# Optimization experiments

Measured on AMD Instinct MI355X. Metric: run time of the kernel, lower is better.

The kernel has to match this reference:

```python
import jax, jax.numpy as jnp
import numpy as np

N_EVENTS = 16
N_SAMPLES = 2 ** 15  # 32768


def fft_shift(stems, shift_samples):
    """Fractionally shift each atom in time via frequency-domain phase rotation.
    stems: (B, E, N) float32; shift_samples: (B, E) float32 in [0, N].
    """
    n = stems.shape[-1]
    freqs = jnp.fft.rfftfreq(n).astype(jnp.float32)  # (n//2+1,) cycles/sample
    theta = 2.0 * jnp.pi * freqs[None, None, :] * shift_samples[..., None]  # (B,E,F)
    phase = jnp.cos(theta) - 1j * jnp.sin(theta)  # exp(-i*theta)
    spec = jnp.fft.rfft(stems, axis=-1)
    return jnp.fft.irfft(spec * phase, n=n, axis=-1)


def setup_inputs() -> dict:
    key = jax.random.key(0)
    k1, k2, k3, k4 = jax.random.split(key, 4)
    B = 64
    time_latent = jax.random.normal(k1, (B, N_EVENTS, 128), dtype=jnp.float32)
    stems = jax.random.normal(k2, (B, N_EVENTS, N_SAMPLES), dtype=jnp.float32)
    targets = jax.random.normal(k3, (B, 1, N_SAMPLES), dtype=jnp.float32)
    W_pos = jax.random.normal(k4, (1, 128), dtype=jnp.float32) * 0.1
    b_pos = jnp.zeros((1,), dtype=jnp.float32)
    return {"time_latent": time_latent, "stems": stems, "targets": targets,
            "W_pos": W_pos, "b_pos": b_pos}


def reference(time_latent, stems, targets, W_pos, b_pos):
    # to_pos: Linear(128 -> 1), then sigmoid -> fractional positions in [0,1]
    pos = jax.nn.sigmoid(jnp.einsum('bed,od->beo', time_latent, W_pos) + b_pos)
    pos = pos.reshape(-1, N_EVENTS)  # (B, E)
    # schedule_atoms: place each stem at fractional offset pos * n_samples, sum events
    shifted = fft_shift(stems, pos * N_SAMPLES)  # (B, E, N)
    scheduled = jnp.sum(shifted, axis=1, keepdims=True)  # (B, 1, N), same shape as targets
    return scheduled
```

## Files before the change

kernel.cpp:

```cpp
#include <hip/hip_runtime.h>
#include <math.h>

#define NS      32768
#define M       16384
#define NEV     16
#define NB      64
#define T2      1024

__device__ __forceinline__ int ldsIdx(int i) { return i + (i >> 5) + (i >> 10); }
#define LDS_ELEMS (M + M / 32 + M / 1024)

__device__ __forceinline__ float2 cmul(float2 a, float2 b) {
    return make_float2(a.x * b.x - a.y * b.y, a.x * b.y + a.y * b.x);
}

__device__ __forceinline__ int rev4_14(int i) {
    int r = 0;
#pragma unroll
    for (int d = 0; d < 7; ++d) { r = (r << 2) | (i & 3); i >>= 2; }
    return r;
}

__device__ __forceinline__ float2 shift_phase(int k, int si, float sf) {
    unsigned ksi = ((unsigned)k * (unsigned)si) & (unsigned)(NS - 1);
    float total = (float)ksi + (float)k * sf;
    float f = total * (1.0f / (float)NS);
    f -= floorf(f);
    float ang = -6.28318530717958647692f * f;
    float sv, cv;
    __sincosf(ang, &sv, &cv);
    return make_float2(cv, sv);
}

__device__ __forceinline__ float2 wNS(int k) {
    float ang = (float)k * (-6.28318530717958647692f / (float)NS);
    float sv, cv;
    __sincosf(ang, &sv, &cv);
    return make_float2(cv, sv);
}

template <int SIGN>
__device__ void fft_lds(float2* lds, int tid) {
#pragma unroll
    for (int t = 0; t < 7; ++t) {
        const int q = 1 << (2 * t);
        const float c = (SIGN < 0 ? -6.28318530717958647692f
                                  :  6.28318530717958647692f) / (float)(4 * q);
#pragma unroll
        for (int it = 0; it < (M / 4) / T2; ++it) {
            const int bf = tid + it * T2;
            const int g = bf >> (2 * t);
            const int j = bf & (q - 1);
            const int base = (g << (2 * t + 2)) + j;
            const int I0 = ldsIdx(base);
            const int I1 = ldsIdx(base + q);
            const int I2 = ldsIdx(base + 2 * q);
            const int I3 = ldsIdx(base + 3 * q);
            float2 a0 = lds[I0];
            float2 a1 = lds[I1];
            float2 a2 = lds[I2];
            float2 a3 = lds[I3];
            if (q != 1) {
                float sv, cv;
                __sincosf(c * (float)j, &sv, &cv);
                float2 w1 = make_float2(cv, sv);
                float2 w2 = cmul(w1, w1);
                float2 w3 = cmul(w2, w1);
                a1 = cmul(a1, w1);
                a2 = cmul(a2, w2);
                a3 = cmul(a3, w3);
            }
            float2 u0 = make_float2(a0.x + a2.x, a0.y + a2.y);
            float2 u1 = make_float2(a0.x - a2.x, a0.y - a2.y);
            float2 u2 = make_float2(a1.x + a3.x, a1.y + a3.y);
            float2 u3 = make_float2(a1.x - a3.x, a1.y - a3.y);
            lds[I0] = make_float2(u0.x + u2.x, u0.y + u2.y);
            lds[I2] = make_float2(u0.x - u2.x, u0.y - u2.y);
            if (SIGN < 0) {
                lds[I1] = make_float2(u1.x + u3.y, u1.y - u3.x);
                lds[I3] = make_float2(u1.x - u3.y, u1.y + u3.x);
            } else {
                lds[I1] = make_float2(u1.x - u3.y, u1.y + u3.x);
                lds[I3] = make_float2(u1.x + u3.y, u1.y - u3.x);
            }
        }
        __syncthreads();
    }
}

__global__ __launch_bounds__(64) void pos_kernel(const float* __restrict__ tl,
                                                 const float* __restrict__ W,
                                                 const float* __restrict__ bp,
                                                 float* __restrict__ shifts) {
    int bid = blockIdx.x;
    int t = threadIdx.x;
    const float* row = tl + (size_t)bid * 128;
    float p = row[t] * W[t] + row[t + 64] * W[t + 64];
#pragma unroll
    for (int off = 32; off > 0; off >>= 1) p += __shfl_down(p, off);
    if (t == 0) {
        float x = p + bp[0];
        float sig = 1.0f / (1.0f + expf(-x));
        shifts[bid] = sig * (float)NS;
    }
}

__global__ __launch_bounds__(T2) void fft_phase_kernel(float* __restrict__ stems,
                                                       const float* __restrict__ shifts) {
    __shared__ float2 lds[LDS_ELEMS];
    const int tid = threadIdx.x;
    const int row = blockIdx.x;

    float* rowp = stems + (size_t)row * NS;
    const float4* src = (const float4*)rowp;
#pragma unroll
    for (int it = 0; it < (M / 2) / T2; ++it) {
        int i = tid + it * T2;
        float4 v = src[i];
        lds[ldsIdx(rev4_14(2 * i))]     = make_float2(v.x, v.y);
        lds[ldsIdx(rev4_14(2 * i + 1))] = make_float2(v.z, v.w);
    }
    __syncthreads();

    fft_lds<-1>(lds, tid);

    const float s = shifts[row];
    const int si = (int)floorf(s);
    const float sf = s - (float)si;
    float2* spec = (float2*)rowp;
#pragma unroll
    for (int t = 0; t < M / T2; ++t) {
        int k = tid + (t << 10);
        if (k == 0) {
            float2 z0 = lds[ldsIdx(0)];
            float X0 = z0.x + z0.y;
            float XM = z0.x - z0.y;
            float2 phM = shift_phase(M, si, sf);
            spec[0] = make_float2(X0, XM * phM.x);
        } else {
            float2 Zk = lds[ldsIdx(k)];
            float2 Zr = lds[ldsIdx(M - k)];
            float2 E = make_float2(0.5f * (Zk.x + Zr.x), 0.5f * (Zk.y - Zr.y));
            float2 O = make_float2(0.5f * (Zk.y + Zr.y), -0.5f * (Zk.x - Zr.x));
            float2 w = wNS(k);
            float2 wo = cmul(w, O);
            float2 X = make_float2(E.x + wo.x, E.y + wo.y);
            float2 ph = shift_phase(k, si, sf);
            spec[k] = cmul(X, ph);
        }
    }
}

__global__ __launch_bounds__(256) void reduce_kernel(const float4* __restrict__ stems,
                                                     float4* __restrict__ out) {
    int gid = blockIdx.x * 256 + threadIdx.x;
    int b = gid >> 13;
    int i = gid & (NS / 4 - 1);
    const float4* base = stems + (size_t)b * NEV * (NS / 4) + i;
    float4 s = base[0];
#pragma unroll
    for (int e = 1; e < NEV; ++e) {
        float4 v = base[(size_t)e * (NS / 4)];
        s.x += v.x; s.y += v.y; s.z += v.z; s.w += v.w;
    }
    out[gid] = s;
}

__global__ __launch_bounds__(T2) void inv_kernel(float* __restrict__ out) {
    __shared__ float2 lds[LDS_ELEMS];
    const int tid = threadIdx.x;
    const int b = blockIdx.x;

    const float4* src = (const float4*)(out + (size_t)b * NS);
#pragma unroll
    for (int it = 0; it < (M / 2) / T2; ++it) {
        int i = tid + it * T2;
        float4 v = src[i];
        lds[ldsIdx(rev4_14(2 * i))]     = make_float2(v.x, v.y);
        lds[ldsIdx(rev4_14(2 * i + 1))] = make_float2(v.z, v.w);
    }
    __syncthreads();

#pragma unroll
    for (int t = 0; t < (M / 2) / T2; ++t) {
        int k = tid + (t << 10);
        if (k == 0) {
            float2 a0 = lds[ldsIdx(0)];
            lds[ldsIdx(0)] = make_float2(0.5f * (a0.x + a0.y), 0.5f * (a0.x - a0.y));
            int rh = ldsIdx(rev4_14(M / 2));
            float2 ah = lds[rh];
            lds[rh] = make_float2(ah.x, -ah.y);
        } else {
            int pk = ldsIdx(rev4_14(k));
            int pm = ldsIdx(rev4_14(M - k));
            float2 a = lds[pk];
            float2 bb = lds[pm];
            float2 w = wNS(k);
            float2 E1 = make_float2(0.5f * (a.x + bb.x), 0.5f * (a.y - bb.y));
            float2 D1 = make_float2(0.5f * (a.x - bb.x), 0.5f * (a.y + bb.y));
            float2 wc = make_float2(w.x, -w.y);
            float2 O1 = cmul(wc, D1);
            float2 z1 = make_float2(E1.x - O1.y, E1.y + O1.x);
            float2 E2 = make_float2(E1.x, -E1.y);
            float2 D2 = make_float2(-D1.x, D1.y);
            float2 O2 = cmul(w, D2);
            O2 = make_float2(-O2.x, -O2.y);
            float2 z2 = make_float2(E2.x - O2.y, E2.y + O2.x);
            lds[pk] = z1;
            lds[pm] = z2;
        }
    }
    __syncthreads();

    fft_lds<1>(lds, tid);

    const float invM = 1.0f / (float)M;
    float4* dst = (float4*)(out + (size_t)b * NS);
#pragma unroll
    for (int it = 0; it < (NS / 4) / T2; ++it) {
        int i = tid + it * T2;
        float2 z0 = lds[ldsIdx(2 * i)];
        float2 z1 = lds[ldsIdx(2 * i + 1)];
        dst[i] = make_float4(z0.x * invM, z0.y * invM, z1.x * invM, z1.y * invM);
    }
}

extern "C" void kernel_launch(void* const* d_in, const int* in_sizes, int n_in,
                              void* d_out, int out_size, void* d_ws, size_t ws_size,
                              hipStream_t stream) {
    const float* time_latent = (const float*)d_in[0];
    float* stems = (float*)d_in[1];
    const float* W_pos = (const float*)d_in[3];
    const float* b_pos = (const float*)d_in[4];
    float* out = (float*)d_out;

    float* shifts = (float*)d_ws;

    pos_kernel<<<NB * NEV, 64, 0, stream>>>(time_latent, W_pos, b_pos, shifts);
    fft_phase_kernel<<<NB * NEV, T2, 0, stream>>>(stems, shifts);
    reduce_kernel<<<(NB * NS / 4) / 256, 256, 0, stream>>>((const float4*)stems,
                                                           (float4*)out);
    inv_kernel<<<NB, T2, 0, stream>>>(out);
}
```

Baseline: 310.5 us.

## Fuse pairs of radix-4 FFT stages into register-resident radix-16 passes

Measured after the change: 296.4 us. 4.5% less time.

```diff
diff --git a/kernel.cpp b/kernel.cpp
--- a/kernel.cpp
+++ b/kernel.cpp
@@ -39,37 +39,108 @@
     return make_float2(cv, sv);
 }
 
+__device__ __constant__ float R16C[4] = {1.0f, 0.92387953251128675613f,
+                                         0.70710678118654752440f, 0.38268343236508977173f};
+__device__ __constant__ float R16S[4] = {0.0f, 0.38268343236508977173f,
+                                         0.70710678118654752440f, 0.92387953251128675613f};
+
 template <int SIGN>
 __device__ void fft_lds(float2* lds, int tid) {
-#pragma unroll
-    for (int t = 0; t < 7; ++t) {
+    const float TP = (SIGN < 0) ? -6.28318530717958647692f
+                                :  6.28318530717958647692f;
+#pragma unroll
+    for (int tp = 0; tp < 3; ++tp) {
+        const int t = 2 * tp;
         const int q = 1 << (2 * t);
-        const float c = (SIGN < 0 ? -6.28318530717958647692f
-                                  :  6.28318530717958647692f) / (float)(4 * q);
+        const int j = tid & (q - 1);
+        const int base = ((tid >> (2 * t)) << (2 * t + 4)) + j;
+        float2 x[16];
+#pragma unroll
+        for (int l = 0; l < 16; ++l) x[l] = lds[ldsIdx(base + l * q)];
+
+        float2 w1, w2, w3;
+        if (tp > 0) {
+            float sv, cv;
+            __sincosf(TP * (float)j / (float)(4 * q), &sv, &cv);
+            w1 = make_float2(cv, sv);
+            w2 = cmul(w1, w1);
+            w3 = cmul(w2, w1);
+        }
+#pragma unroll
+        for (int m = 0; m < 4; ++m) {
+            float2 a0 = x[4 * m], a1 = x[4 * m + 1], a2 = x[4 * m + 2], a3 = x[4 * m + 3];
+            if (tp > 0) { a1 = cmul(a1, w1); a2 = cmul(a2, w2); a3 = cmul(a3, w3); }
+            float2 u0 = make_float2(a0.x + a2.x, a0.y + a2.y);
+            float2 u1 = make_float2(a0.x - a2.x, a0.y - a2.y);
+            float2 u2 = make_float2(a1.x + a3.x, a1.y + a3.y);
+            float2 u3 = make_float2(a1.x - a3.x, a1.y - a3.y);
+            x[4 * m]     = make_float2(u0.x + u2.x, u0.y + u2.y);
+            x[4 * m + 2] = make_float2(u0.x - u2.x, u0.y - u2.y);
+            if (SIGN < 0) {
+                x[4 * m + 1] = make_float2(u1.x + u3.y, u1.y - u3.x);
+                x[4 * m + 3] = make_float2(u1.x - u3.y, u1.y + u3.x);
+            } else {
+                x[4 * m + 1] = make_float2(u1.x - u3.y, u1.y + u3.x);
+                x[4 * m + 3] = make_float2(u1.x + u3.y, u1.y - u3.x);
+            }
+        }
+
+        float2 ww;
+        if (tp > 0) {
+            float sv, cv;
+            __sincosf(TP * (float)j / (float)(16 * q), &sv, &cv);
+            ww = make_float2(cv, sv);
+        }
+#pragma unroll
+        for (int n = 0; n < 4; ++n) {
+            float2 a0 = x[n], a1 = x[n + 4], a2 = x[n + 8], a3 = x[n + 12];
+            if (!(tp == 0 && n == 0)) {
+                float2 r = make_float2(R16C[n], (SIGN < 0) ? -R16S[n] : R16S[n]);
+                float2 wp = (tp > 0) ? ((n > 0) ? cmul(ww, r) : ww) : r;
+                float2 wp2 = cmul(wp, wp);
+                float2 wp3 = cmul(wp2, wp);
+                a1 = cmul(a1, wp);
+                a2 = cmul(a2, wp2);
+                a3 = cmul(a3, wp3);
+            }
+            float2 u0 = make_float2(a0.x + a2.x, a0.y + a2.y);
+            float2 u1 = make_float2(a0.x - a2.x, a0.y - a2.y);
+            float2 u2 = make_float2(a1.x + a3.x, a1.y + a3.y);
+            float2 u3 = make_float2(a1.x - a3.x, a1.y - a3.y);
+            x[n]      = make_float2(u0.x + u2.x, u0.y + u2.y);
+            x[n + 8]  = make_float2(u0.x - u2.x, u0.y - u2.y);
+            if (SIGN < 0) {
+                x[n + 4]  = make_float2(u1.x + u3.y, u1.y - u3.x);
+                x[n + 12] = make_float2(u1.x - u3.y, u1.y + u3.x);
+            } else {
+                x[n + 4]  = make_float2(u1.x - u3.y, u1.y + u3.x);
+                x[n + 12] = make_float2(u1.x + u3.y, u1.y - u3.x);
+            }
+        }
+#pragma unroll
+        for (int l = 0; l < 16; ++l) lds[ldsIdx(base + l * q)] = x[l];
+        __syncthreads();
+    }
+
+    {
+        const int q = 4096;
+        const float c = TP / (float)(4 * q);
 #pragma unroll
         for (int it = 0; it < (M / 4) / T2; ++it) {
-            const int bf = tid + it * T2;
-            const int g = bf >> (2 * t);
-            const int j = bf & (q - 1);
-            const int base = (g << (2 * t + 2)) + j;
-            const int I0 = ldsIdx(base);
-            const int I1 = ldsIdx(base + q);
-            const int I2 = ldsIdx(base + 2 * q);
-            const int I3 = ldsIdx(base + 3 * q);
+            const int j = tid + it * T2;
+            float sv, cv;
+            __sincosf(c * (float)j, &sv, &cv);
+            float2 w1 = make_float2(cv, sv);
+            float2 w2 = cmul(w1, w1);
+            float2 w3 = cmul(w2, w1);
+            const int I0 = ldsIdx(j);
+            const int I1 = ldsIdx(j + q);
+            const int I2 = ldsIdx(j + 2 * q);
+            const int I3 = ldsIdx(j + 3 * q);
             float2 a0 = lds[I0];
-            float2 a1 = lds[I1];
-            float2 a2 = lds[I2];
-            float2 a3 = lds[I3];
-            if (q != 1) {
-                float sv, cv;
-                __sincosf(c * (float)j, &sv, &cv);
-                float2 w1 = make_float2(cv, sv);
-                float2 w2 = cmul(w1, w1);
-                float2 w3 = cmul(w2, w1);
-                a1 = cmul(a1, w1);
-                a2 = cmul(a2, w2);
-                a3 = cmul(a3, w3);
-            }
+            float2 a1 = cmul(lds[I1], w1);
+            float2 a2 = cmul(lds[I2], w2);
+            float2 a3 = cmul(lds[I3], w3);
             float2 u0 = make_float2(a0.x + a2.x, a0.y + a2.y);
             float2 u1 = make_float2(a0.x - a2.x, a0.y - a2.y);
             float2 u2 = make_float2(a1.x + a3.x, a1.y + a3.y);
```
